# Performance work log

Hardware: AMD Instinct MI355X
Metric: run time of the kernel (lower is better)

## Reference

```python
import jax, jax.numpy as jnp
import numpy as np

N_VNS, N_CNS, DV = 8192, 4096, 3      # regular (3,6) LDPC, rate 1/2
BATCH = 1024
NUM_ITER = 20
PHI_MIN, PHI_MAX = 8.5e-08, 16.635532  # clip range of _phi from the module


def _build_edges():
    """Gallager-style regular (dv=3, dc=6) Tanner graph; deduped like a 0/1 pcm."""
    rng = np.random.default_rng(0)
    dc = N_VNS * DV // N_CNS  # 6
    cn = np.concatenate([rng.permutation(np.repeat(np.arange(N_CNS), dc // DV * DV // (dc // DV)))
                         if False else rng.permutation(np.repeat(np.arange(N_CNS), N_VNS // N_CNS))
                         for _ in range(DV)])
    vn = np.tile(np.arange(N_VNS), DV)
    keys = np.unique(cn.astype(np.int64) * N_VNS + vn)  # unique (cn, vn) pairs, sorted by cn
    vn_con = (keys % N_VNS).astype(np.int32)
    cn_con = (keys // N_VNS).astype(np.int32)
    return vn_con, cn_con


def setup_inputs() -> dict:
    key = jax.random.key(0)
    vn_con, cn_con = _build_edges()
    llr_ch = jax.random.normal(key, (BATCH, N_VNS), dtype=jnp.float32) * 2.0
    return {"llr_ch": llr_ch,
            "vn_con": jnp.asarray(vn_con),
            "cn_con": jnp.asarray(cn_con),
            "num_cns": N_CNS}


def _phi(x):
    # phi(x) = log((e^x + 1)/(e^x - 1)), clipped exactly as in the module
    x = jnp.clip(x, PHI_MIN, PHI_MAX)
    return jnp.log(jnp.exp(x) + 1.0) - jnp.log(jnp.exp(x) - 1.0)


def reference(llr_ch, vn_con, cn_con, num_cns):
    num_vns = llr_ch.shape[1]
    # Sionna layout: internal llr [num_vns, batch]; logits -> llr sign flip
    llr = -llr_ch.T
    num_edges = vn_con.shape[0]
    msg0 = jnp.zeros((num_edges, llr.shape[1]), llr.dtype)

    def vn_update(msg):
        # x_{i->j} = llr_i + sum_{j' in N(i)} y_{j'->i} - y_{j->i}
        node_sum = jax.ops.segment_sum(msg, vn_con, num_segments=num_vns) + llr
        return node_sum[vn_con] - msg

    def cn_update(msg):
        # boxplus-phi: sign product (excl. self) * phi(sum phi(|m|) - phi(|m_self|))
        sign = jnp.where(msg == 0.0, 1.0, jnp.sign(msg))
        sign_node = jax.ops.segment_prod(sign, cn_con, num_segments=num_cns)
        sign_out = jax.lax.stop_gradient(sign) * sign_node[cn_con]
        p = _phi(jnp.abs(msg))
        psum = jax.ops.segment_sum(p, cn_con, num_segments=num_cns)
        return sign_out * _phi(psum[cn_con] - p)

    def step(msg, _):
        return cn_update(vn_update(msg)), None

    msg, _ = jax.lax.scan(step, msg0, None, length=NUM_ITER)

    # marginalization + llr -> logits sign flip; soft output (hard_out=False)
    x_tot = llr + jax.ops.segment_sum(msg, vn_con, num_segments=num_vns)
    return (-x_tot).T  # [batch, num_vns]
```

## Files before the change

kernel.cpp:

```cpp
#include <hip/hip_runtime.h>

#define N_VNS   8192
#define N_CNS   4096
#define BATCH   1024
#define NUM_ITER 20
#define MAX_E   24576
#define LOG2E   1.44269504088896f
#define LN2     0.693147180559945f
#define YMAX2   24.0f
#define RCLAMP  0x1.fffffcp-1f
#define LDS_BYTES (MAX_E * 4)

__device__ __forceinline__ float t2T(float t) {
    float tc = fminf(fmaxf(t, -YMAX2), YMAX2);
    float E = __builtin_amdgcn_exp2f(tc);
    float T = (E - 1.0f) * __builtin_amdgcn_rcpf(E + 1.0f);
    return fminf(fmaxf(T, -RCLAMP), RCLAMP);
}

__device__ __forceinline__ float r2m(float r) {
    float rc = fminf(fmaxf(r, -RCLAMP), RCLAMP);
    return __builtin_amdgcn_logf((1.0f + rc) * __builtin_amdgcn_rcpf(1.0f - rc));
}


__global__ void count_edges(const int* __restrict__ vn_con, const int* __restrict__ cn_con,
                            int E, int* __restrict__ vn_cnt, int* __restrict__ cn_cnt) {
    int e = blockIdx.x * 256 + threadIdx.x;
    if (e < E) {
        atomicAdd(&vn_cnt[vn_con[e]], 1);
        atomicAdd(&cn_cnt[cn_con[e]], 1);
    }
}

__global__ void scan_excl(const int* __restrict__ cnt, int n, int* __restrict__ ptr) {
    __shared__ int sh[1024];
    int carry = 0;
    if (threadIdx.x == 0) ptr[0] = 0;
    for (int base = 0; base < n; base += 1024) {
        int i = base + (int)threadIdx.x;
        int v = (i < n) ? cnt[i] : 0;
        sh[threadIdx.x] = v;
        __syncthreads();
        for (int off = 1; off < 1024; off <<= 1) {
            int add = ((int)threadIdx.x >= off) ? sh[threadIdx.x - off] : 0;
            __syncthreads();
            sh[threadIdx.x] += add;
            __syncthreads();
        }
        if (i < n) ptr[i + 1] = carry + sh[threadIdx.x];
        carry += sh[1023];
        __syncthreads();
    }
}

__global__ void fill_vn(const int* __restrict__ vn_con, int E,
                        const int* __restrict__ vn_ptr, int* __restrict__ vn_fill,
                        int* __restrict__ vn_eids) {
    int e = blockIdx.x * 256 + threadIdx.x;
    if (e < E) {
        int v = vn_con[e];
        int slot = atomicAdd(&vn_fill[v], 1);
        vn_eids[vn_ptr[v] + slot] = e;
    }
}

__global__ void sort_pack_vn(const int* __restrict__ vn_ptr, int* __restrict__ vn_eids,
                             const int* __restrict__ cn_con, const int* __restrict__ cn_ptr,
                             uint2* __restrict__ vn_pack) {
    int v = blockIdx.x * 256 + threadIdx.x;
    if (v >= N_VNS) return;
    int s = vn_ptr[v], n = vn_ptr[v + 1] - s;
    for (int i = 1; i < n; ++i) {
        int key = vn_eids[s + i];
        int j = i - 1;
        while (j >= 0 && vn_eids[s + j] > key) { vn_eids[s + j + 1] = vn_eids[s + j]; --j; }
        vn_eids[s + j + 1] = key;
    }
    unsigned sl[3];
    for (int k = 0; k < 3; ++k) {
        sl[k] = 0xFFFFu;
        if (k < n) {
            int eid = vn_eids[s + k];
            int cn = cn_con[eid];
            unsigned rank = (unsigned)(eid - cn_ptr[cn]);
            sl[k] = rank * N_CNS + (unsigned)cn;
        }
    }
    vn_pack[v] = make_uint2(sl[0] | (sl[1] << 16), sl[2] | 0xFFFF0000u);
}

__global__ void pad_assign(const int* __restrict__ cn_ptr, int* __restrict__ pad_cnt,
                           uint2* __restrict__ vn_pack) {
    int c = blockIdx.x * 256 + threadIdx.x;
    if (c >= N_CNS) return;
    int deg = cn_ptr[c + 1] - cn_ptr[c];
    for (int r = deg; r < 6; ++r) {
        int idx = atomicAdd(pad_cnt, 1);
        if (idx < 2048) {
            unsigned slot = (unsigned)r * N_CNS + (unsigned)c;
            vn_pack[idx].y = (vn_pack[idx].y & 0xFFFFu) | (slot << 16);
        }
    }
}


__global__ __launch_bounds__(1024)
__attribute__((amdgpu_waves_per_eu(4, 4)))
void decode(const float* __restrict__ llr_ch, float* __restrict__ out,
            const uint2* __restrict__ vn_pack) {
    extern __shared__ float q[];

    int b = blockIdx.x, tid = threadIdx.x;
    const float* llr_row = llr_ch + (size_t)b * N_VNS;

    float llr[8];
    float Tllr[8];
    uint2 pw[8];
    #pragma unroll
    for (int i = 0; i < 8; ++i) {
        int v = i * 1024 + tid;
        llr[i] = -llr_row[v] * LOG2E;
        pw[i] = vn_pack[v];
    }
    unsigned pad0 = pw[0].y >> 16;
    unsigned pad1 = pw[1].y >> 16;

    #pragma unroll
    for (int k = 0; k < 24; ++k) q[k * 1024 + tid] = 1.0f;
    __syncthreads();
    #pragma unroll
    for (int i = 0; i < 8; ++i) {
        float T0 = t2T(llr[i]);
        Tllr[i] = T0;
        unsigned s0 = pw[i].x & 0xFFFFu, s1 = pw[i].x >> 16, s2 = pw[i].y & 0xFFFFu;
        if (s0 != 0xFFFFu) q[s0] = T0;
        if (s1 != 0xFFFFu) q[s1] = T0;
        if (s2 != 0xFFFFu) q[s2] = T0;
    }
    __syncthreads();

    for (int it = 0; it < NUM_ITER; ++it) {
        #pragma unroll
        for (int i = 0; i < 4; ++i) {
            int c = i * 1024 + tid;
            float T0 = q[c];
            float T1 = q[N_CNS + c];
            float T2 = q[2 * N_CNS + c];
            float T3 = q[3 * N_CNS + c];
            float T4 = q[4 * N_CNS + c];
            float T5 = q[5 * N_CNS + c];
            float p1 = T0 * T1, p2 = p1 * T2, p3 = p2 * T3, p4 = p3 * T4;
            float s4 = T5 * T4, s3 = s4 * T3, s2 = s3 * T2, s1 = s2 * T1;
            q[c]             = s1;
            q[N_CNS + c]     = T0 * s2;
            q[2 * N_CNS + c] = p1 * s3;
            q[3 * N_CNS + c] = p2 * s4;
            q[4 * N_CNS + c] = p3 * T5;
            q[5 * N_CNS + c] = p4;
        }
        __syncthreads();
        if (it == NUM_ITER - 1) break;

        #pragma unroll
        for (int i = 0; i < 8; ++i) {
            unsigned s0 = pw[i].x & 0xFFFFu, s1 = pw[i].x >> 16, s2 = pw[i].y & 0xFFFFu;
            float r0 = 0.f, r1 = 0.f, r2 = 0.f;
            if (s0 != 0xFFFFu) r0 = fminf(fmaxf(q[s0], -RCLAMP), RCLAMP);
            if (s1 != 0xFFFFu) r1 = fminf(fmaxf(q[s1], -RCLAMP), RCLAMP);
            if (s2 != 0xFFFFu) r2 = fminf(fmaxf(q[s2], -RCLAMP), RCLAMP);
            float T = Tllr[i];
            float A12 = __builtin_fmaf(r1, r2, 1.0f), B12 = r1 + r2;
            float A02 = __builtin_fmaf(r0, r2, 1.0f), B02 = r0 + r2;
            float A01 = __builtin_fmaf(r0, r1, 1.0f), B01 = r0 + r1;
            float n0 = __builtin_fmaf(T, A12, B12), d0 = __builtin_fmaf(T, B12, A12);
            float n1 = __builtin_fmaf(T, A02, B02), d1 = __builtin_fmaf(T, B02, A02);
            float n2 = __builtin_fmaf(T, A01, B01), d2 = __builtin_fmaf(T, B01, A01);
            float t0 = n0 * __builtin_amdgcn_rcpf(d0);
            float t1 = n1 * __builtin_amdgcn_rcpf(d1);
            float t2 = n2 * __builtin_amdgcn_rcpf(d2);
            t0 = fminf(fmaxf(t0, -RCLAMP), RCLAMP);
            t1 = fminf(fmaxf(t1, -RCLAMP), RCLAMP);
            t2 = fminf(fmaxf(t2, -RCLAMP), RCLAMP);
            if (s0 != 0xFFFFu) q[s0] = t0;
            if (s1 != 0xFFFFu) q[s1] = t1;
            if (s2 != 0xFFFFu) q[s2] = t2;
        }
        if (pad0 != 0xFFFFu) q[pad0] = 1.0f;
        if (pad1 != 0xFFFFu) q[pad1] = 1.0f;
        __syncthreads();
    }

    float* orow = out + (size_t)b * N_VNS;
    #pragma unroll
    for (int i = 0; i < 8; ++i) {
        unsigned s0 = pw[i].x & 0xFFFFu, s1 = pw[i].x >> 16, s2 = pw[i].y & 0xFFFFu;
        float ns = llr[i];
        if (s0 != 0xFFFFu) ns += r2m(q[s0]);
        if (s1 != 0xFFFFu) ns += r2m(q[s1]);
        if (s2 != 0xFFFFu) ns += r2m(q[s2]);
        orow[i * 1024 + tid] = -ns * LN2;
    }
}

extern "C" void kernel_launch(void* const* d_in, const int* in_sizes, int n_in,
                              void* d_out, int out_size, void* d_ws, size_t ws_size,
                              hipStream_t stream) {
    const float* llr_ch = (const float*)d_in[0];
    const int* vn_con = (const int*)d_in[1];
    const int* cn_con = (const int*)d_in[2];
    int E = in_sizes[1];
    float* out = (float*)d_out;

    char* ws = (char*)d_ws;
    size_t off = 0;
    auto alloc = [&](size_t bytes) -> void* {
        void* ptr = ws + off;
        off = (off + bytes + 255) & ~(size_t)255;
        return ptr;
    };
    int* vn_ptr  = (int*)alloc((N_VNS + 1) * 4);
    int* cn_ptr  = (int*)alloc((N_CNS + 1) * 4);
    int* vn_cnt  = (int*)alloc(N_VNS * 4);
    int* cn_cnt  = (int*)alloc(N_CNS * 4);
    int* vn_fill = (int*)alloc(N_VNS * 4);
    int* vn_eids = (int*)alloc((size_t)E * 4);
    uint2* vn_pack = (uint2*)alloc((size_t)N_VNS * 8);
    int* pad_cnt = (int*)alloc(4);

    hipMemsetAsync(vn_cnt, 0, N_VNS * 4, stream);
    hipMemsetAsync(cn_cnt, 0, N_CNS * 4, stream);
    hipMemsetAsync(vn_fill, 0, N_VNS * 4, stream);
    hipMemsetAsync(pad_cnt, 0, 4, stream);

    count_edges<<<(E + 255) / 256, 256, 0, stream>>>(vn_con, cn_con, E, vn_cnt, cn_cnt);
    scan_excl<<<1, 1024, 0, stream>>>(vn_cnt, N_VNS, vn_ptr);
    scan_excl<<<1, 1024, 0, stream>>>(cn_cnt, N_CNS, cn_ptr);
    fill_vn<<<(E + 255) / 256, 256, 0, stream>>>(vn_con, E, vn_ptr, vn_fill, vn_eids);
    sort_pack_vn<<<(N_VNS + 255) / 256, 256, 0, stream>>>(vn_ptr, vn_eids, cn_con, cn_ptr,
                                                          vn_pack);
    pad_assign<<<(N_CNS + 255) / 256, 256, 0, stream>>>(cn_ptr, pad_cnt, vn_pack);

    static bool attr_set = false;
    if (!attr_set) {
        hipFuncSetAttribute((const void*)decode,
                            hipFuncAttributeMaxDynamicSharedMemorySize, LDS_BYTES);
        attr_set = true;
    }
    decode<<<BATCH, 1024, LDS_BYTES, stream>>>(llr_ch, out, vn_pack);
}
```

Baseline: 352.1 us.

## Interleave CN rank slots for vector LDS access and use branchless dummy-slot addressing

Changes the shared-memory layout so each check node's ranks are stored in interleaved pairs, letting the check-node update use three 64-bit LDS loads and stores instead of six scalar ones. Edge slots are precomputed as byte offsets, with missing edges redirected to a dedicated zero slot, which removes the per-access branches and the clamp on reads in the variable-node phase. The goal is fewer LDS instructions and less branch and unpacking overhead. In exchange it holds 24 address registers per thread, which could raise register pressure, and adds some LDS traffic to the dummy slot.

```diff
diff --git a/kernel.cpp b/kernel.cpp
--- a/kernel.cpp
+++ b/kernel.cpp
@@ -9,7 +9,11 @@
 #define LN2     0.693147180559945f
 #define YMAX2   24.0f
 #define RCLAMP  0x1.fffffcp-1f
-#define LDS_BYTES (MAX_E * 4)
+#define ZSLOT   24576
+#define ZBYTE   (ZSLOT * 4)
+#define LDS_BYTES ((MAX_E + 64) * 4)
+
+typedef float v2f __attribute__((ext_vector_type(2)));
 
 __device__ __forceinline__ float t2T(float t) {
     float tc = fminf(fmaxf(t, -YMAX2), YMAX2);
@@ -21,6 +25,10 @@
 __device__ __forceinline__ float r2m(float r) {
     float rc = fminf(fmaxf(r, -RCLAMP), RCLAMP);
     return __builtin_amdgcn_logf((1.0f + rc) * __builtin_amdgcn_rcpf(1.0f - rc));
+}
+
+__device__ __forceinline__ unsigned qslot(unsigned rank, unsigned cn) {
+    return (rank >> 1) * (2 * N_CNS) + cn * 2 + (rank & 1);
 }
 
 
@@ -84,7 +92,7 @@
             int eid = vn_eids[s + k];
             int cn = cn_con[eid];
             unsigned rank = (unsigned)(eid - cn_ptr[cn]);
-            sl[k] = rank * N_CNS + (unsigned)cn;
+            sl[k] = qslot(rank, (unsigned)cn);
         }
     }
     vn_pack[v] = make_uint2(sl[0] | (sl[1] << 16), sl[2] | 0xFFFF0000u);
@@ -98,7 +106,7 @@
     for (int r = deg; r < 6; ++r) {
         int idx = atomicAdd(pad_cnt, 1);
         if (idx < 2048) {
-            unsigned slot = (unsigned)r * N_CNS + (unsigned)c;
+            unsigned slot = qslot((unsigned)r, (unsigned)c);
             vn_pack[idx].y = (vn_pack[idx].y & 0xFFFFu) | (slot << 16);
         }
     }
@@ -110,65 +118,72 @@
 void decode(const float* __restrict__ llr_ch, float* __restrict__ out,
             const uint2* __restrict__ vn_pack) {
     extern __shared__ float q[];
+    char* qb = (char*)q;
 
     int b = blockIdx.x, tid = threadIdx.x;
     const float* llr_row = llr_ch + (size_t)b * N_VNS;
 
     float llr[8];
     float Tllr[8];
-    uint2 pw[8];
-    #pragma unroll
-    for (int i = 0; i < 8; ++i) {
-        int v = i * 1024 + tid;
-        llr[i] = -llr_row[v] * LOG2E;
-        pw[i] = vn_pack[v];
-    }
-    unsigned pad0 = pw[0].y >> 16;
-    unsigned pad1 = pw[1].y >> 16;
+    unsigned a[8][3];
+    unsigned pad0, pad1;
+    {
+        uint2 pw0 = vn_pack[tid], pw1 = vn_pack[1024 + tid];
+        pad0 = pw0.y >> 16;
+        pad1 = pw1.y >> 16;
+        #pragma unroll
+        for (int i = 0; i < 8; ++i) {
+            int v = i * 1024 + tid;
+            uint2 pw = (i == 0) ? pw0 : (i == 1) ? pw1 : vn_pack[v];
+            llr[i] = -llr_row[v] * LOG2E;
+            Tllr[i] = t2T(llr[i]);
+            unsigned s0 = pw.x & 0xFFFFu, s1 = pw.x >> 16, s2 = pw.y & 0xFFFFu;
+            a[i][0] = (s0 == 0xFFFFu) ? ZBYTE : s0 * 4;
+            a[i][1] = (s1 == 0xFFFFu) ? ZBYTE : s1 * 4;
+            a[i][2] = (s2 == 0xFFFFu) ? ZBYTE : s2 * 4;
+        }
+        pad0 = (pad0 == 0xFFFFu) ? 0xFFFFFFFFu : pad0 * 4;
+        pad1 = (pad1 == 0xFFFFu) ? 0xFFFFFFFFu : pad1 * 4;
+    }
 
     #pragma unroll
     for (int k = 0; k < 24; ++k) q[k * 1024 + tid] = 1.0f;
+    if (tid == 0) q[ZSLOT] = 0.0f;
     __syncthreads();
     #pragma unroll
     for (int i = 0; i < 8; ++i) {
-        float T0 = t2T(llr[i]);
-        Tllr[i] = T0;
-        unsigned s0 = pw[i].x & 0xFFFFu, s1 = pw[i].x >> 16, s2 = pw[i].y & 0xFFFFu;
-        if (s0 != 0xFFFFu) q[s0] = T0;
-        if (s1 != 0xFFFFu) q[s1] = T0;
-        if (s2 != 0xFFFFu) q[s2] = T0;
+        float T0 = Tllr[i];
+        #pragma unroll
+        for (int k = 0; k < 3; ++k)
+            *(float*)(qb + a[i][k]) = (a[i][k] == ZBYTE) ? 0.0f : T0;
     }
     __syncthreads();
 
     for (int it = 0; it < NUM_ITER; ++it) {
         #pragma unroll
         for (int i = 0; i < 4; ++i) {
-            int c = i * 1024 + tid;
-            float T0 = q[c];
-            float T1 = q[N_CNS + c];
-            float T2 = q[2 * N_CNS + c];
-            float T3 = q[3 * N_CNS + c];
-            float T4 = q[4 * N_CNS + c];
-            float T5 = q[5 * N_CNS + c];
+            unsigned c8 = (unsigned)(i * 1024 + tid) * 8u;
+            v2f T01 = *(v2f*)(qb + c8);
+            v2f T23 = *(v2f*)(qb + 32768 + c8);
+            v2f T45 = *(v2f*)(qb + 65536 + c8);
+            float T0 = T01.x, T1 = T01.y, T2 = T23.x, T3 = T23.y, T4 = T45.x, T5 = T45.y;
             float p1 = T0 * T1, p2 = p1 * T2, p3 = p2 * T3, p4 = p3 * T4;
             float s4 = T5 * T4, s3 = s4 * T3, s2 = s3 * T2, s1 = s2 * T1;
-            q[c]             = s1;
-            q[N_CNS + c]     = T0 * s2;
-            q[2 * N_CNS + c] = p1 * s3;
-            q[3 * N_CNS + c] = p2 * s4;
-            q[4 * N_CNS + c] = p3 * T5;
-            q[5 * N_CNS + c] = p4;
+            v2f e01 = { s1, T0 * s2 };
+            v2f e23 = { p1 * s3, p2 * s4 };
+            v2f e45 = { p3 * T5, p4 };
+            *(v2f*)(qb + c8) = e01;
+            *(v2f*)(qb + 32768 + c8) = e23;
+            *(v2f*)(qb + 65536 + c8) = e45;
         }
         __syncthreads();
         if (it == NUM_ITER - 1) break;
 
         #pragma unroll
         for (int i = 0; i < 8; ++i) {
-            unsigned s0 = pw[i].x & 0xFFFFu, s1 = pw[i].x >> 16, s2 = pw[i].y & 0xFFFFu;
-            float r0 = 0.f, r1 = 0.f, r2 = 0.f;
-            if (s0 != 0xFFFFu) r0 = fminf(fmaxf(q[s0], -RCLAMP), RCLAMP);
-            if (s1 != 0xFFFFu) r1 = fminf(fmaxf(q[s1], -RCLAMP), RCLAMP);
-            if (s2 != 0xFFFFu) r2 = fminf(fmaxf(q[s2], -RCLAMP), RCLAMP);
+            float r0 = *(float*)(qb + a[i][0]);
+            float r1 = *(float*)(qb + a[i][1]);
+            float r2 = *(float*)(qb + a[i][2]);
             float T = Tllr[i];
             float A12 = __builtin_fmaf(r1, r2, 1.0f), B12 = r1 + r2;
             float A02 = __builtin_fmaf(r0, r2, 1.0f), B02 = r0 + r2;
@@ -182,23 +197,22 @@
             t0 = fminf(fmaxf(t0, -RCLAMP), RCLAMP);
             t1 = fminf(fmaxf(t1, -RCLAMP), RCLAMP);
             t2 = fminf(fmaxf(t2, -RCLAMP), RCLAMP);
-            if (s0 != 0xFFFFu) q[s0] = t0;
-            if (s1 != 0xFFFFu) q[s1] = t1;
-            if (s2 != 0xFFFFu) q[s2] = t2;
-        }
-        if (pad0 != 0xFFFFu) q[pad0] = 1.0f;
-        if (pad1 != 0xFFFFu) q[pad1] = 1.0f;
+            *(float*)(qb + a[i][0]) = (a[i][0] == ZBYTE) ? 0.0f : t0;
+            *(float*)(qb + a[i][1]) = (a[i][1] == ZBYTE) ? 0.0f : t1;
+            *(float*)(qb + a[i][2]) = (a[i][2] == ZBYTE) ? 0.0f : t2;
+        }
+        if (pad0 != 0xFFFFFFFFu) *(float*)(qb + pad0) = 1.0f;
+        if (pad1 != 0xFFFFFFFFu) *(float*)(qb + pad1) = 1.0f;
         __syncthreads();
     }
 
     float* orow = out + (size_t)b * N_VNS;
     #pragma unroll
     for (int i = 0; i < 8; ++i) {
-        unsigned s0 = pw[i].x & 0xFFFFu, s1 = pw[i].x >> 16, s2 = pw[i].y & 0xFFFFu;
         float ns = llr[i];
-        if (s0 != 0xFFFFu) ns += r2m(q[s0]);
-        if (s1 != 0xFFFFu) ns += r2m(q[s1]);
-        if (s2 != 0xFFFFu) ns += r2m(q[s2]);
+        ns += r2m(*(float*)(qb + a[i][0]));
+        ns += r2m(*(float*)(qb + a[i][1]));
+        ns += r2m(*(float*)(qb + a[i][2]));
         orow[i * 1024 + tid] = -ns * LN2;
     }
 }
```

Measured after the change: 336.9 us. -4.3%, faster.

## Store per-check total product and recover extrinsic by division in VN update

Applied to the files above, without the earlier changes.

The check-node pass now writes a single product of all six tanh-domain messages per check, instead of six leave-one-out products. Each variable node keeps its own outgoing messages in registers and recovers the extrinsic value as total product times the reciprocal of its own message. Messages are clamped away from zero to keep that division safe. The edge-slot layout changes to a 4+2 arrangement so the check pass can use vector LDS loads, and padding is handled through scratch and zero slots, which removes the pad_assign kernel. This cuts LDS writes and multiplies per iteration, at the cost of more registers per thread and some accuracy loss from dividing out a clamped message.

```diff
diff --git a/kernel.cpp b/kernel.cpp
--- a/kernel.cpp
+++ b/kernel.cpp
@@ -7,20 +7,31 @@
 #define MAX_E   24576
 #define LOG2E   1.44269504088896f
 #define LN2     0.693147180559945f
-#define YMAX2   24.0f
 #define RCLAMP  0x1.fffffcp-1f
-#define LDS_BYTES (MAX_E * 4)
+#define TMIN    4.25e-08f
+#define TSCRATCH 24576
+#define PBASE    24640
+#define PZERO    (PBASE + N_CNS)
+#define LDS_WORDS (PZERO + 64)
+#define LDS_BYTES (LDS_WORDS * 4)
+
+typedef float v2f __attribute__((ext_vector_type(2)));
+typedef float v4f __attribute__((ext_vector_type(4)));
 
 __device__ __forceinline__ float t2T(float t) {
-    float tc = fminf(fmaxf(t, -YMAX2), YMAX2);
+    float tc = fminf(fmaxf(t, -24.0f), 24.0f);
     float E = __builtin_amdgcn_exp2f(tc);
-    float T = (E - 1.0f) * __builtin_amdgcn_rcpf(E + 1.0f);
-    return fminf(fmaxf(T, -RCLAMP), RCLAMP);
+    return (E - 1.0f) * __builtin_amdgcn_rcpf(E + 1.0f);
 }
 
 __device__ __forceinline__ float r2m(float r) {
     float rc = fminf(fmaxf(r, -RCLAMP), RCLAMP);
     return __builtin_amdgcn_logf((1.0f + rc) * __builtin_amdgcn_rcpf(1.0f - rc));
+}
+
+__device__ __forceinline__ float guardT(float t) {
+    float m = fminf(fmaxf(fabsf(t), TMIN), RCLAMP);
+    return __builtin_copysignf(m, t);
 }
 
 
@@ -84,24 +95,11 @@
             int eid = vn_eids[s + k];
             int cn = cn_con[eid];
             unsigned rank = (unsigned)(eid - cn_ptr[cn]);
-            sl[k] = rank * N_CNS + (unsigned)cn;
-        }
-    }
-    vn_pack[v] = make_uint2(sl[0] | (sl[1] << 16), sl[2] | 0xFFFF0000u);
-}
-
-__global__ void pad_assign(const int* __restrict__ cn_ptr, int* __restrict__ pad_cnt,
-                           uint2* __restrict__ vn_pack) {
-    int c = blockIdx.x * 256 + threadIdx.x;
-    if (c >= N_CNS) return;
-    int deg = cn_ptr[c + 1] - cn_ptr[c];
-    for (int r = deg; r < 6; ++r) {
-        int idx = atomicAdd(pad_cnt, 1);
-        if (idx < 2048) {
-            unsigned slot = (unsigned)r * N_CNS + (unsigned)c;
-            vn_pack[idx].y = (vn_pack[idx].y & 0xFFFFu) | (slot << 16);
-        }
-    }
+            sl[k] = (rank < 4) ? ((unsigned)cn * 4 + rank)
+                               : (16384u + (unsigned)cn * 2 + (rank - 4));
+        }
+    }
+    vn_pack[v] = make_uint2(sl[0] | (sl[1] << 16), sl[2]);
 }
 
 
@@ -110,65 +108,65 @@
 void decode(const float* __restrict__ llr_ch, float* __restrict__ out,
             const uint2* __restrict__ vn_pack) {
     extern __shared__ float q[];
+    char* qb = (char*)q;
 
     int b = blockIdx.x, tid = threadIdx.x;
     const float* llr_row = llr_ch + (size_t)b * N_VNS;
 
     float llr[8];
     float Tllr[8];
-    uint2 pw[8];
+    float qr[8][3];
+    unsigned aT[8][3];
+    unsigned aP[8][3];
     #pragma unroll
     for (int i = 0; i < 8; ++i) {
         int v = i * 1024 + tid;
+        uint2 pw = vn_pack[v];
         llr[i] = -llr_row[v] * LOG2E;
-        pw[i] = vn_pack[v];
-    }
-    unsigned pad0 = pw[0].y >> 16;
-    unsigned pad1 = pw[1].y >> 16;
+        Tllr[i] = guardT(t2T(llr[i]));
+        unsigned s[3] = { pw.x & 0xFFFFu, pw.x >> 16, pw.y & 0xFFFFu };
+        #pragma unroll
+        for (int k = 0; k < 3; ++k) {
+            unsigned sk = s[k];
+            bool miss = (sk == 0xFFFFu);
+            unsigned cn = (sk < 16384u) ? (sk >> 2) : ((sk - 16384u) >> 1);
+            aT[i][k] = miss ? (TSCRATCH * 4u) : (sk * 4u);
+            aP[i][k] = miss ? (PZERO * 4u) : ((PBASE + cn) * 4u);
+        }
+    }
 
     #pragma unroll
     for (int k = 0; k < 24; ++k) q[k * 1024 + tid] = 1.0f;
+    if (tid == 0) { q[TSCRATCH] = 1.0f; q[PZERO] = 0.0f; }
     __syncthreads();
     #pragma unroll
     for (int i = 0; i < 8; ++i) {
-        float T0 = t2T(llr[i]);
-        Tllr[i] = T0;
-        unsigned s0 = pw[i].x & 0xFFFFu, s1 = pw[i].x >> 16, s2 = pw[i].y & 0xFFFFu;
-        if (s0 != 0xFFFFu) q[s0] = T0;
-        if (s1 != 0xFFFFu) q[s1] = T0;
-        if (s2 != 0xFFFFu) q[s2] = T0;
+        float T0 = Tllr[i];
+        #pragma unroll
+        for (int k = 0; k < 3; ++k) { qr[i][k] = T0; *(float*)(qb + aT[i][k]) = T0; }
     }
     __syncthreads();
 
     for (int it = 0; it < NUM_ITER; ++it) {
         #pragma unroll
         for (int i = 0; i < 4; ++i) {
-            int c = i * 1024 + tid;
-            float T0 = q[c];
-            float T1 = q[N_CNS + c];
-            float T2 = q[2 * N_CNS + c];
-            float T3 = q[3 * N_CNS + c];
-            float T4 = q[4 * N_CNS + c];
-            float T5 = q[5 * N_CNS + c];
-            float p1 = T0 * T1, p2 = p1 * T2, p3 = p2 * T3, p4 = p3 * T4;
-            float s4 = T5 * T4, s3 = s4 * T3, s2 = s3 * T2, s1 = s2 * T1;
-            q[c]             = s1;
-            q[N_CNS + c]     = T0 * s2;
-            q[2 * N_CNS + c] = p1 * s3;
-            q[3 * N_CNS + c] = p2 * s4;
-            q[4 * N_CNS + c] = p3 * T5;
-            q[5 * N_CNS + c] = p4;
+            unsigned c = (unsigned)(i * 1024 + tid);
+            v4f T03 = *(v4f*)(qb + c * 16u);
+            v2f T45 = *(v2f*)(qb + 65536u + c * 8u);
+            float P = ((((T03.x * T03.y) * T03.z) * T03.w) * T45.x) * T45.y;
+            *(float*)(qb + (PBASE * 4u) + c * 4u) = P;
         }
         __syncthreads();
         if (it == NUM_ITER - 1) break;
 
         #pragma unroll
         for (int i = 0; i < 8; ++i) {
-            unsigned s0 = pw[i].x & 0xFFFFu, s1 = pw[i].x >> 16, s2 = pw[i].y & 0xFFFFu;
-            float r0 = 0.f, r1 = 0.f, r2 = 0.f;
-            if (s0 != 0xFFFFu) r0 = fminf(fmaxf(q[s0], -RCLAMP), RCLAMP);
-            if (s1 != 0xFFFFu) r1 = fminf(fmaxf(q[s1], -RCLAMP), RCLAMP);
-            if (s2 != 0xFFFFu) r2 = fminf(fmaxf(q[s2], -RCLAMP), RCLAMP);
+            float P0 = *(float*)(qb + aP[i][0]);
+            float P1 = *(float*)(qb + aP[i][1]);
+            float P2 = *(float*)(qb + aP[i][2]);
+            float r0 = P0 * __builtin_amdgcn_rcpf(qr[i][0]);
+            float r1 = P1 * __builtin_amdgcn_rcpf(qr[i][1]);
+            float r2 = P2 * __builtin_amdgcn_rcpf(qr[i][2]);
             float T = Tllr[i];
             float A12 = __builtin_fmaf(r1, r2, 1.0f), B12 = r1 + r2;
             float A02 = __builtin_fmaf(r0, r2, 1.0f), B02 = r0 + r2;
@@ -176,29 +174,23 @@
             float n0 = __builtin_fmaf(T, A12, B12), d0 = __builtin_fmaf(T, B12, A12);
             float n1 = __builtin_fmaf(T, A02, B02), d1 = __builtin_fmaf(T, B02, A02);
             float n2 = __builtin_fmaf(T, A01, B01), d2 = __builtin_fmaf(T, B01, A01);
-            float t0 = n0 * __builtin_amdgcn_rcpf(d0);
-            float t1 = n1 * __builtin_amdgcn_rcpf(d1);
-            float t2 = n2 * __builtin_amdgcn_rcpf(d2);
-            t0 = fminf(fmaxf(t0, -RCLAMP), RCLAMP);
-            t1 = fminf(fmaxf(t1, -RCLAMP), RCLAMP);
-            t2 = fminf(fmaxf(t2, -RCLAMP), RCLAMP);
-            if (s0 != 0xFFFFu) q[s0] = t0;
-            if (s1 != 0xFFFFu) q[s1] = t1;
-            if (s2 != 0xFFFFu) q[s2] = t2;
-        }
-        if (pad0 != 0xFFFFu) q[pad0] = 1.0f;
-        if (pad1 != 0xFFFFu) q[pad1] = 1.0f;
+            float t0 = guardT(n0 * __builtin_amdgcn_rcpf(d0));
+            float t1 = guardT(n1 * __builtin_amdgcn_rcpf(d1));
+            float t2 = guardT(n2 * __builtin_amdgcn_rcpf(d2));
+            qr[i][0] = t0; *(float*)(qb + aT[i][0]) = t0;
+            qr[i][1] = t1; *(float*)(qb + aT[i][1]) = t1;
+            qr[i][2] = t2; *(float*)(qb + aT[i][2]) = t2;
+        }
         __syncthreads();
     }
 
     float* orow = out + (size_t)b * N_VNS;
     #pragma unroll
     for (int i = 0; i < 8; ++i) {
-        unsigned s0 = pw[i].x & 0xFFFFu, s1 = pw[i].x >> 16, s2 = pw[i].y & 0xFFFFu;
         float ns = llr[i];
-        if (s0 != 0xFFFFu) ns += r2m(q[s0]);
-        if (s1 != 0xFFFFu) ns += r2m(q[s1]);
-        if (s2 != 0xFFFFu) ns += r2m(q[s2]);
+        ns += r2m(*(float*)(qb + aP[i][0]) * __builtin_amdgcn_rcpf(qr[i][0]));
+        ns += r2m(*(float*)(qb + aP[i][1]) * __builtin_amdgcn_rcpf(qr[i][1]));
+        ns += r2m(*(float*)(qb + aP[i][2]) * __builtin_amdgcn_rcpf(qr[i][2]));
         orow[i * 1024 + tid] = -ns * LN2;
     }
 }
@@ -226,12 +218,10 @@
     int* vn_fill = (int*)alloc(N_VNS * 4);
     int* vn_eids = (int*)alloc((size_t)E * 4);
     uint2* vn_pack = (uint2*)alloc((size_t)N_VNS * 8);
-    int* pad_cnt = (int*)alloc(4);
 
     hipMemsetAsync(vn_cnt, 0, N_VNS * 4, stream);
     hipMemsetAsync(cn_cnt, 0, N_CNS * 4, stream);
     hipMemsetAsync(vn_fill, 0, N_VNS * 4, stream);
-    hipMemsetAsync(pad_cnt, 0, 4, stream);
 
     count_edges<<<(E + 255) / 256, 256, 0, stream>>>(vn_con, cn_con, E, vn_cnt, cn_cnt);
     scan_excl<<<1, 1024, 0, stream>>>(vn_cnt, N_VNS, vn_ptr);
@@ -239,7 +229,6 @@
     fill_vn<<<(E + 255) / 256, 256, 0, stream>>>(vn_con, E, vn_ptr, vn_fill, vn_eids);
     sort_pack_vn<<<(N_VNS + 255) / 256, 256, 0, stream>>>(vn_ptr, vn_eids, cn_con, cn_ptr,
                                                           vn_pack);
-    pad_assign<<<(N_CNS + 255) / 256, 256, 0, stream>>>(cn_ptr, pad_cnt, vn_pack);
 
     static bool attr_set = false;
     if (!attr_set) {
```

After: 335.0 us. 4.8% less time.
